# Kernel optimization log

Hardware: AMD Instinct MI355X
Metric: run time of the kernel (lower is better)

## Reference

```python
import jax, jax.numpy as jnp
import numpy as np

N, M, C = 16384, 4096, 32
R = 2.0            # max_neighbour_distance
MULT = 2.0         # neighbor_distance_multiplier
NV = 3             # voxels per axis
TV = NV * NV * NV  # 27 total grid voxels
CH = 128           # query chunk size for kNN
EPS_D = 1e-8
BN_EPS = 1e-5


def _grid_offsets():
    g = jnp.linspace(-R + R / NV, R - R / NV, NV)
    x, y, z = jnp.meshgrid(g, g, g, indexing='ij')
    return jnp.stack([x.ravel(), y.ravel(), z.ravel()], axis=-1)  # (27,3)


def _three_nn(support_xyz, new_xyz, grid_centers):
    """3-NN of each grid center among support points within a cube of half-width
    MULT*R around the parent keypoint (two-step search, neighbor_type=0 cube).
    Returns squared dists (M,27,3), idx (M,27,3), empty (M,)."""
    q = new_xyz.reshape(-1, CH, 3)
    g = grid_centers.reshape(-1, CH, TV, 3)

    def body(args):
        qc, gc = args                                   # (CH,3), (CH,27,3)
        diff = jnp.abs(support_xyz[None, :, :] - qc[:, None, :])   # (CH,N,3)
        cand = jnp.max(diff, axis=-1) <= MULT * R                   # (CH,N)
        d2 = jnp.sum((gc[:, :, None, :] - support_xyz[None, None, :, :]) ** 2,
                     axis=-1)                                       # (CH,27,N)
        d2 = jnp.where(cand[:, None, :], d2, jnp.inf)
        nd, idx = jax.lax.top_k(-d2, 3)                              # (CH,27,3)
        return -nd, idx, ~jnp.any(cand, axis=-1)

    d3, idx, empty = jax.lax.map(body, (q, g))
    d3 = jnp.where(jnp.isinf(d3), 1e10, d3)  # <3 candidates -> ~zero weight
    return (d3.reshape(-1, TV, 3), idx.reshape(-1, TV, 3), empty.reshape(-1))


def _bn_relu(x, gamma, beta):
    mu = jnp.mean(x, axis=0)
    var = jnp.var(x, axis=0)
    return jax.nn.relu((x - mu) * jax.lax.rsqrt(var + BN_EPS) * gamma + beta)


def _forward(support_xyz, support_features, new_xyz,
             w1, bn1_gamma, bn1_beta, w2, bn2_gamma, bn2_beta):
    grid_centers = new_xyz[:, None, :] + _grid_offsets()[None, :, :]  # (M,27,3)
    d3, idx, empty = _three_nn(support_xyz, new_xyz, grid_centers)
    d3 = jax.lax.stop_gradient(d3)  # torch computes kNN under no_grad

    dist_recip = 1.0 / (d3 + EPS_D)                                   # (M,27,3)
    norm = jnp.sum(dist_recip, axis=-1, keepdims=True)
    weight = dist_recip / jnp.maximum(norm, 1e-8)

    nbr_feats = support_features[idx]                 # (M,27,3,C) gather
    interp = jnp.einsum('mgk,mgkc->mgc', weight, nbr_feats)          # (M,27,C)

    nbr_xyz = support_xyz[idx]                        # (M,27,3,3)
    local_xyz = (grid_centers[:, :, None, :] - nbr_xyz).reshape(M, TV, 9)
    feats = jnp.concatenate([interp, local_xyz], axis=-1)            # (M,27,C+9)
    feats = jnp.where(empty[:, None, None], 0.0, feats)

    # grouped Conv1d (kernel 1, groups=27): per-voxel matmul
    y = jnp.einsum('mgc,goc->mgo', feats, w1).reshape(M, TV * 32)     # (M,864)
    y = _bn_relu(y, bn1_gamma, bn1_beta)
    z = y @ w2.T                                                      # (M,128)
    return _bn_relu(z, bn2_gamma, bn2_beta)


def setup_inputs() -> dict:
    key = jax.random.key(0)
    ks = jax.random.split(key, 5)
    scale = jnp.array([50.0, 50.0, 4.0])
    shift = jnp.array([0.0, 0.0, -2.0])
    support_xyz = jax.random.uniform(ks[0], (N, 3)) * scale + shift
    new_xyz = jax.random.uniform(ks[1], (M, 3)) * scale + shift
    support_features = jax.random.normal(ks[2], (N, C))
    w1 = jax.random.normal(ks[3], (TV, 32, C + 9)) * (2.0 / (C + 9)) ** 0.5
    w2 = jax.random.normal(ks[4], (128, TV * 32)) * (2.0 / (TV * 32)) ** 0.5
    return {
        'support_xyz': support_xyz,
        'support_features': support_features,
        'new_xyz': new_xyz,
        'w1': w1,
        'bn1_gamma': jnp.ones(TV * 32),
        'bn1_beta': jnp.zeros(TV * 32),
        'w2': w2,
        'bn2_gamma': jnp.ones(128),
        'bn2_beta': jnp.zeros(128),
    }


def reference(support_xyz, support_features, new_xyz,
              w1, bn1_gamma, bn1_beta, w2, bn2_gamma, bn2_beta):
    return _forward(support_xyz, support_features, new_xyz,
                    w1, bn1_gamma, bn1_beta, w2, bn2_gamma, bn2_beta)
```

## Files before the change

kernel.cpp:

```cpp
#include <hip/hip_runtime.h>
#include <hip/hip_bf16.h>

#define N_SUP 16384
#define M_Q   4096
#define TV    27
#define CIN   41
#define CH1   864
#define CH2   128
#define CAP   1024
#define NB    12

#define C2BM 16
#define C2BN 64
#define C2BK 32

__device__ __forceinline__ float gsel(int i){
  const float GOFF = (float)(-2.0 + 2.0 / 3.0);
  return (i == 0) ? GOFF : ((i == 2) ? -GOFF : 0.0f);
}

__device__ __forceinline__ int binOf(float x){
  int b = (int)(x * (float)(NB / 50.0));
  return (b < 0) ? 0 : ((b > NB - 1) ? NB - 1 : b);
}

__device__ __forceinline__ void insK(unsigned long long key,
                                     unsigned long long& k0,
                                     unsigned long long& k1,
                                     unsigned long long& k2){
  bool b0 = key < k0, b1 = key < k1, b2 = key < k2;
  k2 = b1 ? k1 : (b2 ? key : k2);
  k1 = b0 ? k0 : (b1 ? key : k1);
  k0 = b0 ? key : k0;
}

__global__ void kWT(const float* __restrict__ w1, float* __restrict__ w1T,
                    const float* __restrict__ w2, float* __restrict__ w2T)
{
  int idx = blockIdx.x * 256 + threadIdx.x;
  if (idx < CIN * CH1) {
    int k = idx / CH1, t = idx % CH1;
    w1T[idx] = w1[(size_t)t * CIN + k];
  }
  int j = idx - CIN * CH1;
  if (j >= 0 && j < CH1 * CH2) {
    int k = j / CH2, c = j % CH2;
    w2T[j] = w2[(size_t)c * CH1 + k];
  }
}

__global__ void kCount(const float* __restrict__ sup_xyz, int* __restrict__ counts)
{
  int i = blockIdx.x * 256 + threadIdx.x;
  if (i < N_SUP) {
    float x = sup_xyz[3*i], y = sup_xyz[3*i+1];
    atomicAdd(&counts[binOf(x) * NB + binOf(y)], 1);
  }
}

__global__ void kScan(const int* __restrict__ counts, int* __restrict__ starts, int* __restrict__ cursor)
{
  __shared__ int sc[NB*NB];
  int t = threadIdx.x;
  if (t < NB*NB) sc[t] = counts[t];
  __syncthreads();
  if (t == 0) {
    int acc = 0;
    for (int b = 0; b < NB*NB; b++) { int c = sc[b]; sc[b] = acc; acc += c; }
  }
  __syncthreads();
  if (t < NB*NB) { starts[t] = sc[t]; cursor[t] = sc[t]; }
  if (t == NB*NB) starts[NB*NB] = N_SUP;
}

__global__ void kScatter(const float* __restrict__ sup_xyz, int* __restrict__ cursor,
                         float* __restrict__ xs, float* __restrict__ ys,
                         float* __restrict__ zs, int* __restrict__ sid)
{
  int i = blockIdx.x * 256 + threadIdx.x;
  if (i < N_SUP) {
    float x = sup_xyz[3*i], y = sup_xyz[3*i+1], z = sup_xyz[3*i+2];
    int b = binOf(x) * NB + binOf(y);
    int p = atomicAdd(&cursor[b], 1);
    xs[p] = x; ys[p] = y; zs[p] = z; sid[p] = i;
  }
}

__global__ __launch_bounds__(256) void kA12(const float* __restrict__ xs,
                                            const float* __restrict__ ys,
                                            const float* __restrict__ zs,
                                            const int*   __restrict__ sid,
                                            const int*   __restrict__ starts,
                                            const float* __restrict__ new_xyz,
                                            const float* __restrict__ sup_xyz,
                                            float* __restrict__ nnW,
                                            int*   __restrict__ nnGI,
                                            float* __restrict__ nnLX)
{
  __shared__ float4 cxyz[CAP];
  __shared__ unsigned long long sk[TV][8][3];
  __shared__ int s_cnt;

  const int m   = blockIdx.x;
  const int tid = threadIdx.x;
  if (tid == 0) s_cnt = 0;
  __syncthreads();

  const float qx = new_xyz[m*3+0];
  const float qy = new_xyz[m*3+1];
  const float qz = new_xyz[m*3+2];

  const int bx0 = binOf(qx - 4.0f), bx1 = binOf(qx + 4.0f);
  const int by0 = binOf(qy - 4.0f), by1 = binOf(qy + 4.0f);
  for (int bx = bx0; bx <= bx1; bx++) {
    const int beg = starts[bx * NB + by0];
    const int end = starts[bx * NB + by1 + 1];
    for (int i = beg + tid; i < end; i += 256) {
      float x = xs[i], y = ys[i];
      if (fabsf(__fsub_rn(x, qx)) <= 4.0f && fabsf(__fsub_rn(y, qy)) <= 4.0f) {
        int p = atomicAdd(&s_cnt, 1);
        if (p < CAP) cxyz[p] = make_float4(x, y, zs[i], __uint_as_float((unsigned)sid[i]));
      }
    }
  }
  __syncthreads();
  const int cnt = (s_cnt < CAP) ? s_cnt : CAP;

  const int v = tid >> 3, j = tid & 7;
  if (v < TV) {
    const float gx = qx + gsel(v / 9);
    const float gy = qy + gsel((v / 3) % 3);
    const float gz = qz + gsel(v % 3);
    unsigned long long k0 = ~0ull, k1 = ~0ull, k2 = ~0ull;
    float k2df = __uint_as_float(0xFFFFFFFFu);
    for (int c = j; c < cnt; c += 8) {
      float4 f4 = cxyz[c];
      float dx = __fsub_rn(gx, f4.x);
      float dy = __fsub_rn(gy, f4.y);
      float dz = __fsub_rn(gz, f4.z);
      float dd = __fadd_rn(__fadd_rn(__fmul_rn(dx,dx), __fmul_rn(dy,dy)), __fmul_rn(dz,dz));
      if (!(dd > k2df)) {
        unsigned long long key = ((unsigned long long)__float_as_uint(dd) << 32)
                               | (unsigned long long)__float_as_uint(f4.w);
        insK(key, k0, k1, k2);
        k2df = __uint_as_float((unsigned)(k2 >> 32));
      }
    }
    sk[v][j][0] = k0; sk[v][j][1] = k1; sk[v][j][2] = k2;
  }
  __syncthreads();

  if (tid < TV) {
    const int vv = tid;
    const float gx = qx + gsel(vv / 9);
    const float gy = qy + gsel((vv / 3) % 3);
    const float gz = qz + gsel(vv % 3);
    unsigned long long k0 = ~0ull, k1 = ~0ull, k2 = ~0ull;
    #pragma unroll
    for (int jj = 0; jj < 8; jj++) {
      insK(sk[vv][jj][0], k0, k1, k2);
      insK(sk[vv][jj][1], k0, k1, k2);
      insK(sk[vv][jj][2], k0, k1, k2);
    }
    const int base = m * TV + vv;
    if (cnt > 0) {
      unsigned long long ks[3] = {k0, k1, k2};
      float d[3]; int gi[3]; bool ok[3];
      #pragma unroll
      for (int r = 0; r < 3; r++) {
        unsigned db = (unsigned)(ks[r] >> 32);
        ok[r] = (db != 0xFFFFFFFFu);
        d[r]  = ok[r] ? __uint_as_float(db) : 1e10f;
        gi[r] = ok[r] ? (int)(unsigned)(ks[r] & 0xFFFFFFFFull) : 0;
      }
      float r0 = 1.0f / (d[0] + 1e-8f);
      float r1 = 1.0f / (d[1] + 1e-8f);
      float r2 = 1.0f / (d[2] + 1e-8f);
      float den = fmaxf(r0 + r1 + r2, 1e-8f);
      nnW[base*3+0] = r0 / den; nnW[base*3+1] = r1 / den; nnW[base*3+2] = r2 / den;
      nnGI[base*3+0] = gi[0]; nnGI[base*3+1] = gi[1]; nnGI[base*3+2] = gi[2];
      #pragma unroll
      for (int r = 0; r < 3; r++) {
        if (ok[r]) {
          nnLX[base*9 + r*3 + 0] = gx - sup_xyz[gi[r]*3 + 0];
          nnLX[base*9 + r*3 + 1] = gy - sup_xyz[gi[r]*3 + 1];
          nnLX[base*9 + r*3 + 2] = gz - sup_xyz[gi[r]*3 + 2];
        } else {
          nnLX[base*9 + r*3 + 0] = 0.0f;
          nnLX[base*9 + r*3 + 1] = 0.0f;
          nnLX[base*9 + r*3 + 2] = 0.0f;
        }
      }
    } else {
      #pragma unroll
      for (int r = 0; r < 3; r++) {
        nnW[base*3+r] = 0.0f; nnGI[base*3+r] = 0;
        nnLX[base*9+r*3+0] = 0.0f; nnLX[base*9+r*3+1] = 0.0f; nnLX[base*9+r*3+2] = 0.0f;
      }
    }
  }
}

__global__ __launch_bounds__(256) void kA3(const float* __restrict__ sup_feat,
                                           const float* __restrict__ nnW,
                                           const int*   __restrict__ nnGI,
                                           const float* __restrict__ nnLX,
                                           const float* __restrict__ w1T,
                                           float* __restrict__ y1)
{
  __shared__ float s_feats[8][TV][CIN];
  __shared__ float s_w[8][TV][3];
  __shared__ int   s_gi[8][TV][3];

  const int m0  = blockIdx.x * 8;
  const int tid = threadIdx.x;

  for (int t = tid; t < 8*TV*3; t += 256) {
    int q = t / (TV*3), rem = t % (TV*3);
    s_w[q][rem/3][rem%3]  = nnW[m0*TV*3 + t];
    s_gi[q][rem/3][rem%3] = nnGI[m0*TV*3 + t];
  }
  for (int t = tid; t < 8*TV*9; t += 256) {
    int q = t / (TV*9), rem = t % (TV*9);
    s_feats[q][rem/9][32 + rem%9] = nnLX[m0*TV*9 + t];
  }
  __syncthreads();

  for (int t = tid; t < 8*TV*32; t += 256) {
    const int q = t / (TV*32), rem = t % (TV*32);
    const int v = rem >> 5, ch = rem & 31;
    s_feats[q][v][ch] = s_w[q][v][0] * sup_feat[s_gi[q][v][0]*32 + ch]
                      + s_w[q][v][1] * sup_feat[s_gi[q][v][1]*32 + ch]
                      + s_w[q][v][2] * sup_feat[s_gi[q][v][2]*32 + ch];
  }
  __syncthreads();

  for (int t = tid; t < CH1; t += 256) {
    const int v = t >> 5;
    float acc[8];
    #pragma unroll
    for (int q = 0; q < 8; q++) acc[q] = 0.0f;
    for (int k = 0; k < CIN; k++) {
      float w = w1T[k * CH1 + t];
      #pragma unroll
      for (int q = 0; q < 8; q++) acc[q] += s_feats[q][v][k] * w;
    }
    #pragma unroll
    for (int q = 0; q < 8; q++) y1[(size_t)(m0 + q) * CH1 + t] = acc[q];
  }
}

__global__ void kB(const float* __restrict__ y1, float* __restrict__ stats1)
{
  const int c  = threadIdx.x;
  const int m0 = blockIdx.x * 64;
  float s = 0.0f, ss = 0.0f;
  for (int r = 0; r < 64; r++) {
    float v = y1[(size_t)(m0 + r) * CH1 + c];
    s += v; ss += v * v;
  }
  atomicAdd(&stats1[c],       s);
  atomicAdd(&stats1[CH1 + c], ss);
}

__global__ void kS(const float* __restrict__ stats1,
                   const float* __restrict__ g1, const float* __restrict__ b1,
                   float* __restrict__ scsg, float* __restrict__ shsg)
{
  int c = blockIdx.x * 256 + threadIdx.x;
  if (c < CH1) {
    float s  = stats1[c], ssq = stats1[CH1 + c];
    float mu  = s  * (1.0f / M_Q);
    float var = ssq * (1.0f / M_Q) - mu * mu;
    float r   = 1.0f / sqrtf(var + 1e-5f);
    float gg = g1[c];
    scsg[c] = r * gg;
    shsg[c] = b1[c] - mu * r * gg;
  }
}

__global__ __launch_bounds__(256) void kC(const float* __restrict__ y1,
                                          const float* __restrict__ scsg,
                                          const float* __restrict__ shsg,
                                          const float* __restrict__ w2T,
                                          float* __restrict__ z,
                                          float* __restrict__ stats2)
{
  __shared__ float As[C2BK][21];
  __shared__ float Bs[C2BK][C2BN];
  __shared__ float st_s[2][C2BN];

  const int tid = threadIdx.x;
  const int m0  = (blockIdx.x >> 1) * C2BM;
  const int bn0 = (blockIdx.x & 1) * C2BN;

  if (tid < 2*C2BN) st_s[tid >> 6][tid & 63] = 0.0f;

  const int arow = tid >> 4;
  const int akp  = (tid & 15) * 2;
  const int bkk = tid >> 3;
  const int bc8 = (tid & 7) * 8;
  const int ty = tid >> 5;
  const int tx = tid & 31;

  float2 pa  = *(const float2*)&y1[(size_t)(m0 + arow) * CH1 + akp];
  float2 psc = *(const float2*)&scsg[akp];
  float2 psh = *(const float2*)&shsg[akp];
  float4 pb0 = *(const float4*)&w2T[(size_t)bkk * CH2 + bn0 + bc8];
  float4 pb1 = *(const float4*)&w2T[(size_t)bkk * CH2 + bn0 + bc8 + 4];

  float a00 = 0.f, a01 = 0.f, a10 = 0.f, a11 = 0.f;

  for (int k0 = 0; k0 < CH1; k0 += C2BK) {
    __syncthreads();
    As[akp  ][arow] = fmaxf(pa.x * psc.x + psh.x, 0.0f);
    As[akp+1][arow] = fmaxf(pa.y * psc.y + psh.y, 0.0f);
    *(float4*)&Bs[bkk][bc8]     = pb0;
    *(float4*)&Bs[bkk][bc8 + 4] = pb1;
    __syncthreads();
    const int kn = k0 + C2BK;
    if (kn < CH1) {
      pa  = *(const float2*)&y1[(size_t)(m0 + arow) * CH1 + kn + akp];
      psc = *(const float2*)&scsg[kn + akp];
      psh = *(const float2*)&shsg[kn + akp];
      pb0 = *(const float4*)&w2T[(size_t)(kn + bkk) * CH2 + bn0 + bc8];
      pb1 = *(const float4*)&w2T[(size_t)(kn + bkk) * CH2 + bn0 + bc8 + 4];
    }
    #pragma unroll
    for (int kk = 0; kk < C2BK; kk++) {
      float2 av = *(const float2*)&As[kk][ty*2];
      float2 bv = *(const float2*)&Bs[kk][tx*2];
      a00 += av.x*bv.x; a01 += av.x*bv.y;
      a10 += av.y*bv.x; a11 += av.y*bv.y;
    }
  }

  *(float2*)&z[(size_t)(m0 + ty*2    ) * CH2 + bn0 + tx*2] = make_float2(a00, a01);
  *(float2*)&z[(size_t)(m0 + ty*2 + 1) * CH2 + bn0 + tx*2] = make_float2(a10, a11);

  atomicAdd(&st_s[0][tx*2    ], a00 + a10);
  atomicAdd(&st_s[0][tx*2 + 1], a01 + a11);
  atomicAdd(&st_s[1][tx*2    ], a00*a00 + a10*a10);
  atomicAdd(&st_s[1][tx*2 + 1], a01*a01 + a11*a11);
  __syncthreads();
  if (tid < 2*C2BN) {
    int which = tid >> 6, c = tid & 63;
    int copy = (blockIdx.x >> 1) & 7;
    atomicAdd(&stats2[copy*256 + which*128 + bn0 + c], st_s[which][c]);
  }
}

__global__ void kD(const float* __restrict__ z,
                   const float* __restrict__ stats2,
                   const float* __restrict__ g2,
                   const float* __restrict__ b2,
                   float* __restrict__ out)
{
  int t = blockIdx.x * 256 + threadIdx.x;
  if (t >= M_Q * CH2) return;
  int c = t & 127;
  float s = 0.0f, ss = 0.0f;
  #pragma unroll
  for (int k = 0; k < 8; k++) {
    s  += stats2[k * 256 + c];
    ss += stats2[k * 256 + 128 + c];
  }
  float mu  = s  * (1.0f / M_Q);
  float var = ss * (1.0f / M_Q) - mu * mu;
  float r   = 1.0f / sqrtf(var + 1e-5f);
  float val = fmaxf((z[t] - mu) * r * g2[c] + b2[c], 0.0f);
  out[t] = val;
}

extern "C" void kernel_launch(void* const* d_in, const int* in_sizes, int n_in,
                              void* d_out, int out_size, void* d_ws, size_t ws_size,
                              hipStream_t stream)
{
  const float* sup_xyz  = (const float*)d_in[0];
  const float* sup_feat = (const float*)d_in[1];
  const float* new_xyz  = (const float*)d_in[2];
  const float* w1       = (const float*)d_in[3];
  const float* g1       = (const float*)d_in[4];
  const float* b1       = (const float*)d_in[5];
  const float* w2       = (const float*)d_in[6];
  const float* g2       = (const float*)d_in[7];
  const float* b2       = (const float*)d_in[8];
  float* out = (float*)d_out;

  char* ws = (char*)d_ws;
  float* y1     = (float*)(ws);
  float* z      = (float*)(ws + 14155776);
  float* w2T    = (float*)(ws + 16252928);
  float* stats  = (float*)(ws + 16695296);
  int*   counts = (int*)  (ws + 16710400);
  int*   cursor = (int*)  (ws + 16710976);
  int*   starts = (int*)  (ws + 16711552);
  float* xs     = (float*)(ws + 16712132);
  float* ys     = (float*)(ws + 16777668);
  float* zs     = (float*)(ws + 16843204);
  int*   sid    = (int*)  (ws + 16908740);
  float* nnW    = (float*)(ws + 16974276);
  int*   nnGI   = (int*)  (ws + 18301380);
  float* nnLX   = (float*)(ws + 19628484);
  float* stats1 = stats;
  float* stats2 = stats + 2 * CH1;
  float* w1T    = z;
  float* scsg   = xs;
  float* shsg   = ys;

  hipMemsetAsync(stats, 0, 15104 + 576 + 576, stream);

  const int WT_TOT = CIN*CH1 + CH1*CH2;
  hipLaunchKernelGGL(kWT,     dim3((WT_TOT + 255) / 256), dim3(256), 0, stream, w1, w1T, w2, w2T);
  hipLaunchKernelGGL(kCount,  dim3((N_SUP + 255) / 256),  dim3(256), 0, stream, sup_xyz, counts);
  hipLaunchKernelGGL(kScan,   dim3(1),                    dim3(256), 0, stream, counts, starts, cursor);
  hipLaunchKernelGGL(kScatter,dim3((N_SUP + 255) / 256),  dim3(256), 0, stream, sup_xyz, cursor, xs, ys, zs, sid);
  hipLaunchKernelGGL(kA12,    dim3(M_Q),                  dim3(256), 0, stream, xs, ys, zs, sid, starts, new_xyz, sup_xyz, nnW, nnGI, nnLX);
  hipLaunchKernelGGL(kA3,     dim3(M_Q / 8),              dim3(256), 0, stream, sup_feat, nnW, nnGI, nnLX, w1T, y1);
  hipLaunchKernelGGL(kB,      dim3(M_Q / 64),             dim3(CH1), 0, stream, y1, stats1);
  hipLaunchKernelGGL(kS,      dim3((CH1 + 255) / 256),    dim3(256), 0, stream, stats1, g1, b1, scsg, shsg);
  hipLaunchKernelGGL(kC,      dim3((M_Q / C2BM) * 2),     dim3(256), 0, stream, y1, scsg, shsg, w2T, z, stats2);
  hipLaunchKernelGGL(kD,      dim3((M_Q*CH2 + 255) / 256),dim3(256), 0, stream, z, stats2, g2, b2, out);
}
```

Before: 163.6 us.

## Sort kNN candidates into distance rings for early-exit search; fuse count into weight transpose

Candidates gathered per query are bucketed by integer squared distance to the query (a counting sort into 48 rings in shared memory). Each voxel's scan then stops once a ring's lower bound exceeds a triangle-inequality bound derived from its current 3rd-nearest distance, skipping far candidates. The bin-count kernel is also merged into the weight-transpose kernel to drop one launch. In exchange, candidate collection does two passes over the bins with extra atomics and a serial ring scan, and support ids are packed into 14 bits. The per-lane early break with strided lanes may also cost some exactness.

```diff
diff --git a/kernel.cpp b/kernel.cpp
--- a/kernel.cpp
+++ b/kernel.cpp
@@ -9,6 +9,7 @@
 #define CH2   128
 #define CAP   1024
 #define NB    12
+#define NRING 48
 
 #define C2BM 16
 #define C2BN 64
@@ -22,6 +23,14 @@
 __device__ __forceinline__ int binOf(float x){
   int b = (int)(x * (float)(NB / 50.0));
   return (b < 0) ? 0 : ((b > NB - 1) ? NB - 1 : b);
+}
+
+__device__ __forceinline__ int ringOf(float qx, float qy, float qz,
+                                      float x, float y, float z){
+  float dx = __fsub_rn(qx, x), dy = __fsub_rn(qy, y), dz = __fsub_rn(qz, z);
+  float dq2 = __fadd_rn(__fadd_rn(__fmul_rn(dx,dx), __fmul_rn(dy,dy)), __fmul_rn(dz,dz));
+  int r = (int)dq2;
+  return (r > NRING-1) ? NRING-1 : r;
 }
 
 __device__ __forceinline__ void insK(unsigned long long key,
@@ -34,10 +43,15 @@
   k0 = b0 ? key : k0;
 }
 
-__global__ void kWT(const float* __restrict__ w1, float* __restrict__ w1T,
-                    const float* __restrict__ w2, float* __restrict__ w2T)
+__global__ void kPre(const float* __restrict__ w1, float* __restrict__ w1T,
+                     const float* __restrict__ w2, float* __restrict__ w2T,
+                     const float* __restrict__ sup_xyz, int* __restrict__ counts)
 {
   int idx = blockIdx.x * 256 + threadIdx.x;
+  if (idx < N_SUP) {
+    float x = sup_xyz[3*idx], y = sup_xyz[3*idx+1];
+    atomicAdd(&counts[binOf(x) * NB + binOf(y)], 1);
+  }
   if (idx < CIN * CH1) {
     int k = idx / CH1, t = idx % CH1;
     w1T[idx] = w1[(size_t)t * CIN + k];
@@ -46,15 +60,6 @@
   if (j >= 0 && j < CH1 * CH2) {
     int k = j / CH2, c = j % CH2;
     w2T[j] = w2[(size_t)c * CH1 + k];
-  }
-}
-
-__global__ void kCount(const float* __restrict__ sup_xyz, int* __restrict__ counts)
-{
-  int i = blockIdx.x * 256 + threadIdx.x;
-  if (i < N_SUP) {
-    float x = sup_xyz[3*i], y = sup_xyz[3*i+1];
-    atomicAdd(&counts[binOf(x) * NB + binOf(y)], 1);
   }
 }
 
@@ -97,13 +102,15 @@
                                             int*   __restrict__ nnGI,
                                             float* __restrict__ nnLX)
 {
-  __shared__ float4 cxyz[CAP];
+  __shared__ float4 sxyz[CAP];
+  __shared__ int rbeg[NRING + 1];
+  __shared__ int rcnt[NRING];
+  __shared__ int rcur[NRING];
   __shared__ unsigned long long sk[TV][8][3];
-  __shared__ int s_cnt;
 
   const int m   = blockIdx.x;
   const int tid = threadIdx.x;
-  if (tid == 0) s_cnt = 0;
+  if (tid < NRING) rcnt[tid] = 0;
   __syncthreads();
 
   const float qx = new_xyz[m*3+0];
@@ -112,38 +119,68 @@
 
   const int bx0 = binOf(qx - 4.0f), bx1 = binOf(qx + 4.0f);
   const int by0 = binOf(qy - 4.0f), by1 = binOf(qy + 4.0f);
+
   for (int bx = bx0; bx <= bx1; bx++) {
     const int beg = starts[bx * NB + by0];
     const int end = starts[bx * NB + by1 + 1];
     for (int i = beg + tid; i < end; i += 256) {
       float x = xs[i], y = ys[i];
       if (fabsf(__fsub_rn(x, qx)) <= 4.0f && fabsf(__fsub_rn(y, qy)) <= 4.0f) {
-        int p = atomicAdd(&s_cnt, 1);
-        if (p < CAP) cxyz[p] = make_float4(x, y, zs[i], __uint_as_float((unsigned)sid[i]));
-      }
-    }
-  }
-  __syncthreads();
-  const int cnt = (s_cnt < CAP) ? s_cnt : CAP;
+        atomicAdd(&rcnt[ringOf(qx,qy,qz, x,y,zs[i])], 1);
+      }
+    }
+  }
+  __syncthreads();
+  if (tid == 0) {
+    int acc = 0;
+    #pragma unroll
+    for (int r = 0; r < NRING; r++) { rbeg[r] = acc; rcur[r] = acc; acc += rcnt[r]; }
+    rbeg[NRING] = acc;
+  }
+  __syncthreads();
+  for (int bx = bx0; bx <= bx1; bx++) {
+    const int beg = starts[bx * NB + by0];
+    const int end = starts[bx * NB + by1 + 1];
+    for (int i = beg + tid; i < end; i += 256) {
+      float x = xs[i], y = ys[i];
+      if (fabsf(__fsub_rn(x, qx)) <= 4.0f && fabsf(__fsub_rn(y, qy)) <= 4.0f) {
+        float z = zs[i];
+        int r = ringOf(qx,qy,qz, x,y,z);
+        int p = atomicAdd(&rcur[r], 1);
+        if (p < CAP)
+          sxyz[p] = make_float4(x, y, z,
+                     __uint_as_float(((unsigned)r << 14) | (unsigned)sid[i]));
+      }
+    }
+  }
+  __syncthreads();
+  const int cnt = (rbeg[NRING] < CAP) ? rbeg[NRING] : CAP;
 
   const int v = tid >> 3, j = tid & 7;
   if (v < TV) {
-    const float gx = qx + gsel(v / 9);
-    const float gy = qy + gsel((v / 3) % 3);
-    const float gz = qz + gsel(v % 3);
+    const float ox = gsel(v / 9), oy = gsel((v / 3) % 3), oz = gsel(v % 3);
+    const float gx = qx + ox, gy = qy + oy, gz = qz + oz;
+    const float dgq = sqrtf(ox*ox + oy*oy + oz*oz) + 1e-3f;
+
     unsigned long long k0 = ~0ull, k1 = ~0ull, k2 = ~0ull;
     float k2df = __uint_as_float(0xFFFFFFFFu);
+    float T    = k2df;
     for (int c = j; c < cnt; c += 8) {
-      float4 f4 = cxyz[c];
+      float4 f4 = sxyz[c];
+      unsigned wb = __float_as_uint(f4.w);
+      float E = (float)(wb >> 14);
+      if (E > T) break;
       float dx = __fsub_rn(gx, f4.x);
       float dy = __fsub_rn(gy, f4.y);
       float dz = __fsub_rn(gz, f4.z);
       float dd = __fadd_rn(__fadd_rn(__fmul_rn(dx,dx), __fmul_rn(dy,dy)), __fmul_rn(dz,dz));
       if (!(dd > k2df)) {
         unsigned long long key = ((unsigned long long)__float_as_uint(dd) << 32)
-                               | (unsigned long long)__float_as_uint(f4.w);
+                               | (unsigned long long)(wb & 0x3FFFu);
         insK(key, k0, k1, k2);
         k2df = __uint_as_float((unsigned)(k2 >> 32));
+        float s3 = sqrtf(k2df);
+        T = (dgq + s3) * (dgq + s3) * 1.00001f + 1e-5f;
       }
     }
     sk[v][j][0] = k0; sk[v][j][1] = k1; sk[v][j][2] = k2;
@@ -171,7 +208,7 @@
         unsigned db = (unsigned)(ks[r] >> 32);
         ok[r] = (db != 0xFFFFFFFFu);
         d[r]  = ok[r] ? __uint_as_float(db) : 1e10f;
-        gi[r] = ok[r] ? (int)(unsigned)(ks[r] & 0xFFFFFFFFull) : 0;
+        gi[r] = ok[r] ? (int)(unsigned)(ks[r] & 0x3FFFull) : 0;
       }
       float r0 = 1.0f / (d[0] + 1e-8f);
       float r1 = 1.0f / (d[1] + 1e-8f);
@@ -410,9 +447,8 @@
 
   hipMemsetAsync(stats, 0, 15104 + 576 + 576, stream);
 
-  const int WT_TOT = CIN*CH1 + CH1*CH2;
-  hipLaunchKernelGGL(kWT,     dim3((WT_TOT + 255) / 256), dim3(256), 0, stream, w1, w1T, w2, w2T);
-  hipLaunchKernelGGL(kCount,  dim3((N_SUP + 255) / 256),  dim3(256), 0, stream, sup_xyz, counts);
+  const int PRE_TOT = CIN*CH1 + CH1*CH2;
+  hipLaunchKernelGGL(kPre,    dim3((PRE_TOT + 255) / 256), dim3(256), 0, stream, w1, w1T, w2, w2T, sup_xyz, counts);
   hipLaunchKernelGGL(kScan,   dim3(1),                    dim3(256), 0, stream, counts, starts, cursor);
   hipLaunchKernelGGL(kScatter,dim3((N_SUP + 255) / 256),  dim3(256), 0, stream, sup_xyz, cursor, xs, ys, zs, sid);
   hipLaunchKernelGGL(kA12,    dim3(M_Q),                  dim3(256), 0, stream, xs, ys, zs, sid, starts, new_xyz, sup_xyz, nnW, nnGI, nnLX);
```

Result: slower. 177.8 us (+8.7%).

## Split kNN candidates into near/far sets and prune far scan with sphere bound

Applied to the files above, without the earlier changes.

Candidates in the cube are split into a near set (within 3.75 of the query) stored at the front of shared memory and a far set stored at the back. The 8-way parallel 3-NN scan now covers only the near set. A single thread per voxel scans the far set serially, and only when the triangle-inequality bound cannot prove the near result is exact. The count kernel is also merged into the weight-transpose kernel to save a launch. The risk is that the serial far scan becomes a slow tail when the bound check fails often.

```diff
diff --git a/kernel.cpp b/kernel.cpp
--- a/kernel.cpp
+++ b/kernel.cpp
@@ -9,6 +9,7 @@
 #define CH2   128
 #define CAP   1024
 #define NB    12
+#define NEAR2 14.0625f
 
 #define C2BM 16
 #define C2BN 64
@@ -34,10 +35,15 @@
   k0 = b0 ? key : k0;
 }
 
-__global__ void kWT(const float* __restrict__ w1, float* __restrict__ w1T,
-                    const float* __restrict__ w2, float* __restrict__ w2T)
+__global__ void kPre(const float* __restrict__ w1, float* __restrict__ w1T,
+                     const float* __restrict__ w2, float* __restrict__ w2T,
+                     const float* __restrict__ sup_xyz, int* __restrict__ counts)
 {
   int idx = blockIdx.x * 256 + threadIdx.x;
+  if (idx < N_SUP) {
+    float x = sup_xyz[3*idx], y = sup_xyz[3*idx+1];
+    atomicAdd(&counts[binOf(x) * NB + binOf(y)], 1);
+  }
   if (idx < CIN * CH1) {
     int k = idx / CH1, t = idx % CH1;
     w1T[idx] = w1[(size_t)t * CIN + k];
@@ -46,15 +52,6 @@
   if (j >= 0 && j < CH1 * CH2) {
     int k = j / CH2, c = j % CH2;
     w2T[j] = w2[(size_t)c * CH1 + k];
-  }
-}
-
-__global__ void kCount(const float* __restrict__ sup_xyz, int* __restrict__ counts)
-{
-  int i = blockIdx.x * 256 + threadIdx.x;
-  if (i < N_SUP) {
-    float x = sup_xyz[3*i], y = sup_xyz[3*i+1];
-    atomicAdd(&counts[binOf(x) * NB + binOf(y)], 1);
   }
 }
 
@@ -99,11 +96,11 @@
 {
   __shared__ float4 cxyz[CAP];
   __shared__ unsigned long long sk[TV][8][3];
-  __shared__ int s_cnt;
+  __shared__ int s_nc, s_fc;
 
   const int m   = blockIdx.x;
   const int tid = threadIdx.x;
-  if (tid == 0) s_cnt = 0;
+  if (tid == 0) { s_nc = 0; s_fc = 0; }
   __syncthreads();
 
   const float qx = new_xyz[m*3+0];
@@ -117,14 +114,28 @@
     const int end = starts[bx * NB + by1 + 1];
     for (int i = beg + tid; i < end; i += 256) {
       float x = xs[i], y = ys[i];
-      if (fabsf(__fsub_rn(x, qx)) <= 4.0f && fabsf(__fsub_rn(y, qy)) <= 4.0f) {
-        int p = atomicAdd(&s_cnt, 1);
-        if (p < CAP) cxyz[p] = make_float4(x, y, zs[i], __uint_as_float((unsigned)sid[i]));
-      }
-    }
-  }
-  __syncthreads();
-  const int cnt = (s_cnt < CAP) ? s_cnt : CAP;
+      float dx = __fsub_rn(x, qx), dy = __fsub_rn(y, qy);
+      if (fabsf(dx) <= 4.0f && fabsf(dy) <= 4.0f) {
+        float z = zs[i];
+        float dz = __fsub_rn(z, qz);
+        float dq2 = __fadd_rn(__fadd_rn(__fmul_rn(dx,dx), __fmul_rn(dy,dy)), __fmul_rn(dz,dz));
+        float4 val = make_float4(x, y, z, __uint_as_float((unsigned)sid[i]));
+        if (dq2 <= NEAR2) {
+          int p = atomicAdd(&s_nc, 1);
+          if (p < CAP) cxyz[p] = val;
+        } else {
+          int p = atomicAdd(&s_fc, 1);
+          int idx2 = CAP - 1 - p;
+          if (idx2 >= 0) cxyz[idx2] = val;
+        }
+      }
+    }
+  }
+  __syncthreads();
+  const int ncnt = (s_nc < CAP) ? s_nc : CAP;
+  const int fcnt = (s_fc < CAP) ? s_fc : CAP;
+  const int cnt  = ncnt + fcnt;
+  const int farBeg = CAP - fcnt;
 
   const int v = tid >> 3, j = tid & 7;
   if (v < TV) {
@@ -133,7 +144,7 @@
     const float gz = qz + gsel(v % 3);
     unsigned long long k0 = ~0ull, k1 = ~0ull, k2 = ~0ull;
     float k2df = __uint_as_float(0xFFFFFFFFu);
-    for (int c = j; c < cnt; c += 8) {
+    for (int c = j; c < ncnt; c += 8) {
       float4 f4 = cxyz[c];
       float dx = __fsub_rn(gx, f4.x);
       float dy = __fsub_rn(gy, f4.y);
@@ -152,9 +163,10 @@
 
   if (tid < TV) {
     const int vv = tid;
-    const float gx = qx + gsel(vv / 9);
-    const float gy = qy + gsel((vv / 3) % 3);
-    const float gz = qz + gsel(vv % 3);
+    const float ox = gsel(vv / 9), oy = gsel((vv / 3) % 3), oz = gsel(vv % 3);
+    const float gx = qx + ox, gy = qy + oy, gz = qz + oz;
+    const float dgq = sqrtf(ox*ox + oy*oy + oz*oz) + 1e-3f;
+
     unsigned long long k0 = ~0ull, k1 = ~0ull, k2 = ~0ull;
     #pragma unroll
     for (int jj = 0; jj < 8; jj++) {
@@ -162,6 +174,23 @@
       insK(sk[vv][jj][1], k0, k1, k2);
       insK(sk[vv][jj][2], k0, k1, k2);
     }
+    float k2df = __uint_as_float((unsigned)(k2 >> 32));
+    if (!(sqrtf(k2df) * 1.00002f + dgq <= 3.7498f)) {
+      for (int c = farBeg; c < CAP; c++) {
+        float4 f4 = cxyz[c];
+        float dx = __fsub_rn(gx, f4.x);
+        float dy = __fsub_rn(gy, f4.y);
+        float dz = __fsub_rn(gz, f4.z);
+        float dd = __fadd_rn(__fadd_rn(__fmul_rn(dx,dx), __fmul_rn(dy,dy)), __fmul_rn(dz,dz));
+        if (!(dd > k2df)) {
+          unsigned long long key = ((unsigned long long)__float_as_uint(dd) << 32)
+                                 | (unsigned long long)__float_as_uint(f4.w);
+          insK(key, k0, k1, k2);
+          k2df = __uint_as_float((unsigned)(k2 >> 32));
+        }
+      }
+    }
+
     const int base = m * TV + vv;
     if (cnt > 0) {
       unsigned long long ks[3] = {k0, k1, k2};
@@ -410,9 +439,8 @@
 
   hipMemsetAsync(stats, 0, 15104 + 576 + 576, stream);
 
-  const int WT_TOT = CIN*CH1 + CH1*CH2;
-  hipLaunchKernelGGL(kWT,     dim3((WT_TOT + 255) / 256), dim3(256), 0, stream, w1, w1T, w2, w2T);
-  hipLaunchKernelGGL(kCount,  dim3((N_SUP + 255) / 256),  dim3(256), 0, stream, sup_xyz, counts);
+  const int PRE_TOT = CIN*CH1 + CH1*CH2;
+  hipLaunchKernelGGL(kPre,    dim3((PRE_TOT + 255) / 256), dim3(256), 0, stream, w1, w1T, w2, w2T, sup_xyz, counts);
   hipLaunchKernelGGL(kScan,   dim3(1),                    dim3(256), 0, stream, counts, starts, cursor);
   hipLaunchKernelGGL(kScatter,dim3((N_SUP + 255) / 256),  dim3(256), 0, stream, sup_xyz, cursor, xs, ys, zs, sid);
   hipLaunchKernelGGL(kA12,    dim3(M_Q),                  dim3(256), 0, stream, xs, ys, zs, sid, starts, new_xyz, sup_xyz, nnW, nnGI, nnLX);
```

New measurement: 179.4 us. 1.1x slower.

## Fuse BN1 stats into kA3, merge count into weight transpose, vectorize kD

Applied to the files above, without the earlier changes.

Moves the first batch-norm statistic accumulation into the kA3 epilogue. Each block atomically adds per-channel sums into one of 8 striped copies, which kS then reduces, so the separate kB pass that re-read the 14MB y1 is gone. The support-point bin counting is merged into the weight-transpose kernel, saving a launch. kD now processes float4 vectors. Costs are many more global atomics from kA3 (512 blocks × 864 channels × 2) and a larger memset region.

```diff
diff --git a/kernel.cpp b/kernel.cpp
--- a/kernel.cpp
+++ b/kernel.cpp
@@ -34,10 +34,15 @@
   k0 = b0 ? key : k0;
 }
 
-__global__ void kWT(const float* __restrict__ w1, float* __restrict__ w1T,
-                    const float* __restrict__ w2, float* __restrict__ w2T)
+__global__ void kPre(const float* __restrict__ w1, float* __restrict__ w1T,
+                     const float* __restrict__ w2, float* __restrict__ w2T,
+                     const float* __restrict__ sup_xyz, int* __restrict__ counts)
 {
   int idx = blockIdx.x * 256 + threadIdx.x;
+  if (idx < N_SUP) {
+    float x = sup_xyz[3*idx], y = sup_xyz[3*idx+1];
+    atomicAdd(&counts[binOf(x) * NB + binOf(y)], 1);
+  }
   if (idx < CIN * CH1) {
     int k = idx / CH1, t = idx % CH1;
     w1T[idx] = w1[(size_t)t * CIN + k];
@@ -46,15 +51,6 @@
   if (j >= 0 && j < CH1 * CH2) {
     int k = j / CH2, c = j % CH2;
     w2T[j] = w2[(size_t)c * CH1 + k];
-  }
-}
-
-__global__ void kCount(const float* __restrict__ sup_xyz, int* __restrict__ counts)
-{
-  int i = blockIdx.x * 256 + threadIdx.x;
-  if (i < N_SUP) {
-    float x = sup_xyz[3*i], y = sup_xyz[3*i+1];
-    atomicAdd(&counts[binOf(x) * NB + binOf(y)], 1);
   }
 }
 
@@ -206,7 +202,8 @@
                                            const int*   __restrict__ nnGI,
                                            const float* __restrict__ nnLX,
                                            const float* __restrict__ w1T,
-                                           float* __restrict__ y1)
+                                           float* __restrict__ y1,
+                                           float* __restrict__ stats1)
 {
   __shared__ float s_feats[8][TV][CIN];
   __shared__ float s_w[8][TV][3];
@@ -235,6 +232,7 @@
   }
   __syncthreads();
 
+  const int copy = (blockIdx.x & 7) * 2 * CH1;
   for (int t = tid; t < CH1; t += 256) {
     const int v = t >> 5;
     float acc[8];
@@ -245,22 +243,15 @@
       #pragma unroll
       for (int q = 0; q < 8; q++) acc[q] += s_feats[q][v][k] * w;
     }
+    float s = 0.0f, ss = 0.0f;
     #pragma unroll
-    for (int q = 0; q < 8; q++) y1[(size_t)(m0 + q) * CH1 + t] = acc[q];
-  }
-}
-
-__global__ void kB(const float* __restrict__ y1, float* __restrict__ stats1)
-{
-  const int c  = threadIdx.x;
-  const int m0 = blockIdx.x * 64;
-  float s = 0.0f, ss = 0.0f;
-  for (int r = 0; r < 64; r++) {
-    float v = y1[(size_t)(m0 + r) * CH1 + c];
-    s += v; ss += v * v;
-  }
-  atomicAdd(&stats1[c],       s);
-  atomicAdd(&stats1[CH1 + c], ss);
+    for (int q = 0; q < 8; q++) {
+      y1[(size_t)(m0 + q) * CH1 + t] = acc[q];
+      s += acc[q]; ss += acc[q] * acc[q];
+    }
+    atomicAdd(&stats1[copy + t],       s);
+    atomicAdd(&stats1[copy + CH1 + t], ss);
+  }
 }
 
 __global__ void kS(const float* __restrict__ stats1,
@@ -269,7 +260,12 @@
 {
   int c = blockIdx.x * 256 + threadIdx.x;
   if (c < CH1) {
-    float s  = stats1[c], ssq = stats1[CH1 + c];
+    float s = 0.0f, ssq = 0.0f;
+    #pragma unroll
+    for (int k = 0; k < 8; k++) {
+      s   += stats1[k * 2 * CH1 + c];
+      ssq += stats1[k * 2 * CH1 + CH1 + c];
+    }
     float mu  = s  * (1.0f / M_Q);
     float var = ssq * (1.0f / M_Q) - mu * mu;
     float r   = 1.0f / sqrtf(var + 1e-5f);
@@ -356,20 +352,38 @@
                    const float* __restrict__ b2,
                    float* __restrict__ out)
 {
-  int t = blockIdx.x * 256 + threadIdx.x;
-  if (t >= M_Q * CH2) return;
-  int c = t & 127;
-  float s = 0.0f, ss = 0.0f;
+  int t4 = blockIdx.x * 256 + threadIdx.x;
+  if (t4 >= M_Q * CH2 / 4) return;
+  int c = (t4 & 31) * 4;
+  float4 zv = *(const float4*)&z[(size_t)t4 * 4];
+  float4 sv = make_float4(0,0,0,0), qv = make_float4(0,0,0,0);
   #pragma unroll
   for (int k = 0; k < 8; k++) {
-    s  += stats2[k * 256 + c];
-    ss += stats2[k * 256 + 128 + c];
-  }
-  float mu  = s  * (1.0f / M_Q);
-  float var = ss * (1.0f / M_Q) - mu * mu;
-  float r   = 1.0f / sqrtf(var + 1e-5f);
-  float val = fmaxf((z[t] - mu) * r * g2[c] + b2[c], 0.0f);
-  out[t] = val;
+    float4 a = *(const float4*)&stats2[k * 256 + c];
+    float4 b = *(const float4*)&stats2[k * 256 + 128 + c];
+    sv.x += a.x; sv.y += a.y; sv.z += a.z; sv.w += a.w;
+    qv.x += b.x; qv.y += b.y; qv.z += b.z; qv.w += b.w;
+  }
+  float4 gv = *(const float4*)&g2[c];
+  float4 bv = *(const float4*)&b2[c];
+  float4 o;
+  {
+    float mu = sv.x * (1.0f/M_Q), var = qv.x * (1.0f/M_Q) - mu*mu;
+    o.x = fmaxf((zv.x - mu) * (1.0f/sqrtf(var + 1e-5f)) * gv.x + bv.x, 0.0f);
+  }
+  {
+    float mu = sv.y * (1.0f/M_Q), var = qv.y * (1.0f/M_Q) - mu*mu;
+    o.y = fmaxf((zv.y - mu) * (1.0f/sqrtf(var + 1e-5f)) * gv.y + bv.y, 0.0f);
+  }
+  {
+    float mu = sv.z * (1.0f/M_Q), var = qv.z * (1.0f/M_Q) - mu*mu;
+    o.z = fmaxf((zv.z - mu) * (1.0f/sqrtf(var + 1e-5f)) * gv.z + bv.z, 0.0f);
+  }
+  {
+    float mu = sv.w * (1.0f/M_Q), var = qv.w * (1.0f/M_Q) - mu*mu;
+    o.w = fmaxf((zv.w - mu) * (1.0f/sqrtf(var + 1e-5f)) * gv.w + bv.w, 0.0f);
+  }
+  *(float4*)&out[(size_t)t4 * 4] = o;
 }
 
 extern "C" void kernel_launch(void* const* d_in, const int* in_sizes, int n_in,
@@ -391,34 +405,31 @@
   float* y1     = (float*)(ws);
   float* z      = (float*)(ws + 14155776);
   float* w2T    = (float*)(ws + 16252928);
-  float* stats  = (float*)(ws + 16695296);
-  int*   counts = (int*)  (ws + 16710400);
-  int*   cursor = (int*)  (ws + 16710976);
-  int*   starts = (int*)  (ws + 16711552);
-  float* xs     = (float*)(ws + 16712132);
-  float* ys     = (float*)(ws + 16777668);
-  float* zs     = (float*)(ws + 16843204);
-  int*   sid    = (int*)  (ws + 16908740);
-  float* nnW    = (float*)(ws + 16974276);
-  int*   nnGI   = (int*)  (ws + 18301380);
-  float* nnLX   = (float*)(ws + 19628484);
-  float* stats1 = stats;
-  float* stats2 = stats + 2 * CH1;
+  float* stats1 = (float*)(ws + 16695296);
+  float* stats2 = (float*)(ws + 16750592);
+  int*   counts = (int*)  (ws + 16758784);
+  int*   cursor = (int*)  (ws + 16759360);
+  int*   starts = (int*)  (ws + 16759936);
+  float* xs     = (float*)(ws + 16760516);
+  float* ys     = (float*)(ws + 16826052);
+  float* zs     = (float*)(ws + 16891588);
+  int*   sid    = (int*)  (ws + 16957124);
+  float* nnW    = (float*)(ws + 17022660);
+  int*   nnGI   = (int*)  (ws + 18349764);
+  float* nnLX   = (float*)(ws + 19676868);
   float* w1T    = z;
   float* scsg   = xs;
   float* shsg   = ys;
 
-  hipMemsetAsync(stats, 0, 15104 + 576 + 576, stream);
-
-  const int WT_TOT = CIN*CH1 + CH1*CH2;
-  hipLaunchKernelGGL(kWT,     dim3((WT_TOT + 255) / 256), dim3(256), 0, stream, w1, w1T, w2, w2T);
-  hipLaunchKernelGGL(kCount,  dim3((N_SUP + 255) / 256),  dim3(256), 0, stream, sup_xyz, counts);
+  hipMemsetAsync(stats1, 0, 55296 + 8192 + 576 + 576, stream);
+
+  const int PRE_TOT = CIN*CH1 + CH1*CH2;
+  hipLaunchKernelGGL(kPre,    dim3((PRE_TOT + 255) / 256), dim3(256), 0, stream, w1, w1T, w2, w2T, sup_xyz, counts);
   hipLaunchKernelGGL(kScan,   dim3(1),                    dim3(256), 0, stream, counts, starts, cursor);
   hipLaunchKernelGGL(kScatter,dim3((N_SUP + 255) / 256),  dim3(256), 0, stream, sup_xyz, cursor, xs, ys, zs, sid);
   hipLaunchKernelGGL(kA12,    dim3(M_Q),                  dim3(256), 0, stream, xs, ys, zs, sid, starts, new_xyz, sup_xyz, nnW, nnGI, nnLX);
-  hipLaunchKernelGGL(kA3,     dim3(M_Q / 8),              dim3(256), 0, stream, sup_feat, nnW, nnGI, nnLX, w1T, y1);
-  hipLaunchKernelGGL(kB,      dim3(M_Q / 64),             dim3(CH1), 0, stream, y1, stats1);
+  hipLaunchKernelGGL(kA3,     dim3(M_Q / 8),              dim3(256), 0, stream, sup_feat, nnW, nnGI, nnLX, w1T, y1, stats1);
   hipLaunchKernelGGL(kS,      dim3((CH1 + 255) / 256),    dim3(256), 0, stream, stats1, g1, b1, scsg, shsg);
   hipLaunchKernelGGL(kC,      dim3((M_Q / C2BM) * 2),     dim3(256), 0, stream, y1, scsg, shsg, w2T, z, stats2);
-  hipLaunchKernelGGL(kD,      dim3((M_Q*CH2 + 255) / 256),dim3(256), 0, stream, z, stats2, g2, b2, out);
-}
+  hipLaunchKernelGGL(kD,      dim3(M_Q * CH2 / 4 / 256),  dim3(256), 0, stream, z, stats2, g2, b2, out);
+}
```

Measured after the change: 156.6 us. 4.3% less time.
